# Kernel tuning notes

Measured on AMD Instinct MI355X. Metric: run time of the kernel, lower is better.

The kernel has to match this reference:

```python
import jax, jax.numpy as jnp
import numpy as np

B, N, C = 8, 4096, 768
H, M = 12, 64          # num_heads, num_landmarks
D = C // H             # head_dim = 64


def setup_inputs() -> dict:
    key = jax.random.key(0)
    k1, k2, k3, k4 = jax.random.split(key, 4)
    s = 0.02
    return {
        "x": jax.random.normal(k1, (B, N, C), dtype=jnp.float32),
        "w_qkv": jax.random.normal(k2, (3 * C, C), dtype=jnp.float32) * s,
        "w_proj": jax.random.normal(k3, (C, C), dtype=jnp.float32) * s,
        "b_proj": jax.random.normal(k4, (C,), dtype=jnp.float32) * s,
    }


def iterative_inv(mat, n_iter=6):
    # mat: [B, H, M, M]; Newton-Schulz cubic iteration for pseudo-inverse
    I = jnp.eye(mat.shape[-1], dtype=mat.dtype)
    K = mat
    # init: K^T / max_j(sum_i K_ij)  per (B,H)
    scale = jnp.max(jnp.sum(K, axis=-2), axis=-1)[:, :, None, None]
    V = jnp.swapaxes(K, -1, -2) / scale
    for _ in range(n_iter):
        KV = K @ V
        V = 0.25 * V @ (13.0 * I - KV @ (15.0 * I - KV @ (7.0 * I - KV)))
    return V


def reference(x, w_qkv, w_proj, b_proj):
    b, n, c = x.shape
    qkv = (x @ w_qkv.T).reshape(b, n, 3, H, D).transpose(2, 0, 3, 1, 4)  # [3,B,H,N,D]
    Q, K, V = qkv[0], qkv[1], qkv[2]
    Q = Q / (D ** 0.5)
    # landmark pooling (N % M == 0 path): segment means of length N//M
    Kl = K.reshape(b, H, M, n // M, D).mean(axis=-2)  # [B,H,M,D]
    Ql = Q.reshape(b, H, M, n // M, D).mean(axis=-2)  # [B,H,M,D]
    kernel1 = jax.nn.softmax(jnp.einsum('bhnd,bhmd->bhnm', Q, Kl), axis=-1)   # [B,H,N,M]
    kernel2 = jax.nn.softmax(jnp.einsum('bhmd,bhld->bhml', Ql, Kl), axis=-1)  # [B,H,M,M]
    kernel3 = jax.nn.softmax(jnp.einsum('bhmd,bhnd->bhmn', Ql, K), axis=-1)   # [B,H,M,N]
    SV = (kernel1 @ iterative_inv(kernel2)) @ (kernel3 @ V)  # [B,H,N,D]
    SV = SV.transpose(0, 2, 1, 3).reshape(b, n, c)
    out = SV @ w_proj.T + b_proj
    out = out + V.transpose(0, 2, 1, 3).reshape(b, n, c)
    return out
```

## Files before the change

### kernel.cpp

```cpp
#include <hip/hip_runtime.h>
#include <hip/hip_bf16.h>
#include <stdint.h>

typedef __bf16 bf16;
typedef __bf16 bf16x8 __attribute__((ext_vector_type(8)));
typedef __bf16 bf16x4 __attribute__((ext_vector_type(4)));
typedef float f32x4 __attribute__((ext_vector_type(4)));

#define B_ 8
#define N_ 4096
#define C_ 768
#define H_ 12
#define M_ 64
#define D_ 64
#define NT_ 32768
#define C3_ 2304

typedef __attribute__((address_space(3))) void lds_void_t;
typedef const __attribute__((address_space(1))) void gvoid_t;

__device__ __forceinline__ void gl_lds16(const void* gsrc, void* ldst) {
  __builtin_amdgcn_global_load_lds((gvoid_t*)(uintptr_t)gsrc,
                                   (lds_void_t*)(uintptr_t)ldst, 16, 0, 0);
}

__device__ __forceinline__ f32x4 mfma16(bf16x8 a, bf16x8 b, f32x4 c) {
  return __builtin_amdgcn_mfma_f32_16x16x32_bf16(a, b, c, 0, 0, 0);
}

#define VMW8 asm volatile("s_waitcnt vmcnt(8)" ::: "memory")
#define VMW4 asm volatile("s_waitcnt vmcnt(4)" ::: "memory")
#define VMW0 asm volatile("s_waitcnt vmcnt(0)" ::: "memory")
#define RAWBAR() { __builtin_amdgcn_sched_barrier(0); __builtin_amdgcn_s_barrier(); __builtin_amdgcn_sched_barrier(0); }

__global__ void k_cvt(const float* __restrict__ in, bf16* __restrict__ out, int n4) {
  const int stride = gridDim.x * blockDim.x;
  for (int i = blockIdx.x * blockDim.x + threadIdx.x; i < n4; i += stride) {
    f32x4 v = *(const f32x4*)(in + (size_t)i * 4);
    bf16x4 o;
    o[0] = (bf16)v[0]; o[1] = (bf16)v[1]; o[2] = (bf16)v[2]; o[3] = (bf16)v[3];
    *(bf16x4*)(out + (size_t)i * 4) = o;
  }
}

__global__ __launch_bounds__(512, 2) void k_qkv(
    const bf16* __restrict__ xbf, const bf16* __restrict__ wbf,
    bf16* __restrict__ Qb, bf16* __restrict__ Kb, bf16* __restrict__ Vb,
    float* __restrict__ Qlf, float* __restrict__ Klf)
{
  __shared__ bf16 As[4][8192];
  __shared__ bf16 Bs[4][8192];
  const int t = threadIdx.x;
  const int wave = t >> 6, lane = t & 63;
  const int l15 = lane & 15, l16 = lane >> 4;

  const int bid = blockIdx.x;
  const int swz = (bid & 7) * 144 + (bid >> 3);
  const int bt = swz / 9, ct = swz % 9;
  const int row0 = bt * 256, ct0 = ct * 256;
  const int wr = wave >> 2, wc = wave & 3;

  const int srow = t >> 2;
  const int scol = (((t & 3) ^ ((t >> 3) & 3)) << 3);
  const bf16* gaBase = xbf + (size_t)(row0 + srow) * C_ + scol;
  const bf16* gbBase = wbf + (size_t)(ct0 + srow) * C_ + scol;

  const int aoff = (wr * 128 + l15) * 32 + ((l16 ^ ((l15 >> 1) & 3)) << 3);
  const int boff = (wc * 64 + l15) * 32 + ((l16 ^ ((l15 >> 1) & 3)) << 3);

  f32x4 acc[8][4] = {};
  bf16x8 afr0[4], afr1[4], bfr[2][4];

#define QSTAGE(kt3) {                                                            \
    const int sb_ = (kt3) & 3;                                                   \
    gl_lds16(gaBase + (kt3) * 32, &As[sb_][t * 8]);                              \
    gl_lds16(gbBase + (kt3) * 32, &Bs[sb_][t * 8]);                              \
    gl_lds16(gaBase + (size_t)128 * C_ + (kt3) * 32, &As[sb_][(t + 512) * 8]);   \
    gl_lds16(gbBase + (size_t)128 * C_ + (kt3) * 32, &Bs[sb_][(t + 512) * 8]); }

#define QKSTEP(kt, DO_STAGE, DO_NXT, VMW_, DO_BAR) {                             \
    if (DO_STAGE) QSTAGE((kt) + 3);                                             \
    { const bf16* asC = As[(kt) & 3];                                            \
      _Pragma("unroll")                                                          \
      for (int i = 0; i < 4; ++i)                                                \
        afr1[i] = *(const bf16x8*)&asC[aoff + (4 + i) * 512]; }                  \
    __builtin_amdgcn_s_setprio(1);                                               \
    _Pragma("unroll")                                                            \
    for (int i = 0; i < 4; ++i)                                                  \
      _Pragma("unroll")                                                          \
      for (int j = 0; j < 4; ++j)                                                \
        acc[i][j] = mfma16(afr0[i], bfr[(kt) & 1][j], acc[i][j]);                \
    __builtin_amdgcn_s_setprio(0);                                               \
    if (DO_NXT) {                                                                \
      const bf16* asN = As[((kt) + 1) & 3];                                      \
      const bf16* bsN = Bs[((kt) + 1) & 3];                                      \
      _Pragma("unroll")                                                          \
      for (int i = 0; i < 4; ++i)                                                \
        afr0[i] = *(const bf16x8*)&asN[aoff + i * 512];                          \
      _Pragma("unroll")                                                          \
      for (int j = 0; j < 4; ++j)                                                \
        bfr[((kt) + 1) & 1][j] = *(const bf16x8*)&bsN[boff + j * 512]; }         \
    __builtin_amdgcn_s_setprio(1);                                               \
    _Pragma("unroll")                                                            \
    for (int i = 0; i < 4; ++i)                                                  \
      _Pragma("unroll")                                                          \
      for (int j = 0; j < 4; ++j)                                                \
        acc[4 + i][j] = mfma16(afr1[i], bfr[(kt) & 1][j], acc[4 + i][j]);        \
    __builtin_amdgcn_s_setprio(0);                                               \
    VMW_;                                                                        \
    if (DO_BAR) RAWBAR(); }

  QSTAGE(0); QSTAGE(1); QSTAGE(2);
  VMW4;
  RAWBAR();
#pragma unroll
  for (int i = 0; i < 4; ++i) afr0[i] = *(const bf16x8*)&As[0][aoff + i * 512];
#pragma unroll
  for (int j = 0; j < 4; ++j) bfr[0][j] = *(const bf16x8*)&Bs[0][boff + j * 512];

  QKSTEP(0, 1, 1, VMW4, 1)  QKSTEP(1, 1, 1, VMW4, 1)  QKSTEP(2, 1, 1, VMW4, 1)
  QKSTEP(3, 1, 1, VMW4, 1)  QKSTEP(4, 1, 1, VMW4, 1)  QKSTEP(5, 1, 1, VMW4, 1)
  QKSTEP(6, 1, 1, VMW4, 1)  QKSTEP(7, 1, 1, VMW4, 1)  QKSTEP(8, 1, 1, VMW4, 1)
  QKSTEP(9, 1, 1, VMW4, 1)  QKSTEP(10, 1, 1, VMW4, 1) QKSTEP(11, 1, 1, VMW4, 1)
  QKSTEP(12, 1, 1, VMW4, 1) QKSTEP(13, 1, 1, VMW4, 1) QKSTEP(14, 1, 1, VMW4, 1)
  QKSTEP(15, 1, 1, VMW4, 1) QKSTEP(16, 1, 1, VMW4, 1) QKSTEP(17, 1, 1, VMW4, 1)
  QKSTEP(18, 1, 1, VMW4, 1) QKSTEP(19, 1, 1, VMW4, 1) QKSTEP(20, 1, 1, VMW4, 1)
  QKSTEP(21, 0, 1, VMW0, 1)
  QKSTEP(22, 0, 1, (void)0, 1)
  QKSTEP(23, 0, 0, (void)0, 0)

#undef QKSTEP
#undef QSTAGE

  const int colblock = ct0 + wc * 64;
  const int which = colblock / C_;
  const int h = (colblock % C_) / D_;
  const int b = row0 >> 12;
  const int n_base = (row0 & (N_ - 1)) + wr * 128;
  bf16* dst = (which == 0) ? Qb : (which == 1) ? Kb : Vb;
  const float scale = (which == 0) ? 0.125f : 1.0f;
  const size_t base = ((size_t)(b * H_ + h) * N_ + n_base) * D_;
#pragma unroll
  for (int i = 0; i < 8; ++i)
#pragma unroll
    for (int q = 0; q < 4; ++q) {
      const int rloc = i * 16 + l16 * 4 + q;
#pragma unroll
      for (int j = 0; j < 4; ++j) {
        const int d = j * 16 + l15;
        dst[base + (size_t)rloc * D_ + d] = (bf16)(acc[i][j][q] * scale);
      }
    }
  if (which < 2) {
    float* lmout = (which == 0) ? Qlf : Klf;
#pragma unroll
    for (int g = 0; g < 2; ++g) {
      const int m = (n_base >> 6) + g;
#pragma unroll
      for (int j = 0; j < 4; ++j) {
        float s = 0.f;
#pragma unroll
        for (int i = 4 * g; i < 4 * g + 4; ++i)
#pragma unroll
          for (int q = 0; q < 4; ++q) s += acc[i][j][q];
        s *= scale;
        s += __shfl_xor(s, 16);
        s += __shfl_xor(s, 32);
        if (l16 == 0)
          lmout[((size_t)(b * H_ + h) * M_ + m) * D_ + j * 16 + lane] = s * (1.0f / 64.0f);
      }
    }
  }
}

__global__ __launch_bounds__(512, 1) void k_inv(
    const float* __restrict__ Qlf, const float* __restrict__ Klf,
    float* __restrict__ pinv, bf16* __restrict__ Qlb, bf16* __restrict__ Klb)
{
  __shared__ float K2[4096];
  __shared__ float Vm[4096];
  __shared__ float KV[4096];
  __shared__ float T1[4096];
  __shared__ float U1[4096];
  __shared__ float tmp64[64];
  __shared__ float sscale;
  const int t = threadIdx.x;
  const int bh = blockIdx.x;
  const size_t off = (size_t)bh * 4096;
  for (int idx = t; idx < 4096; idx += 512) {
    const float q = Qlf[off + idx];
    T1[idx] = q;
    Qlb[off + idx] = (bf16)q;
  }
  for (int idx = t; idx < 4096; idx += 512) {
    const int r = idx >> 6, c = idx & 63;
    const float k = Klf[off + idx];
    U1[c * 64 + r] = k;
    Klb[off + idx] = (bf16)k;
  }
  __syncthreads();
  const int j0 = (t & 15) * 4;
  const int i0 = (t >> 4) * 2;

  auto MMstep = [&](const float* A, const float* Bm, float* O, float dg, float sg, float al) {
    float r2[2][4] = {};
    for (int k = 0; k < 64; ++k) {
      f32x4 bv = *(const f32x4*)&Bm[k * 64 + j0];
      const float a0 = A[(i0 + 0) * 64 + k];
      const float a1 = A[(i0 + 1) * 64 + k];
#pragma unroll
      for (int jj = 0; jj < 4; ++jj) { r2[0][jj] += a0 * bv[jj]; r2[1][jj] += a1 * bv[jj]; }
    }
#pragma unroll
    for (int ii = 0; ii < 2; ++ii)
#pragma unroll
      for (int jj = 0; jj < 4; ++jj)
        O[(i0 + ii) * 64 + j0 + jj] = al * (dg * A[(i0 + ii) * 64 + (j0 + jj)] + sg * r2[ii][jj]);
    __syncthreads();
  };

  {
    float r2[2][4] = {};
    for (int k = 0; k < 64; ++k) {
      f32x4 bv = *(const f32x4*)&U1[k * 64 + j0];
      const float a0 = T1[(i0 + 0) * 64 + k];
      const float a1 = T1[(i0 + 1) * 64 + k];
#pragma unroll
      for (int jj = 0; jj < 4; ++jj) { r2[0][jj] += a0 * bv[jj]; r2[1][jj] += a1 * bv[jj]; }
    }
#pragma unroll
    for (int ii = 0; ii < 2; ++ii)
#pragma unroll
      for (int jj = 0; jj < 4; ++jj)
        K2[(i0 + ii) * 64 + j0 + jj] = __expf(r2[ii][jj]);
  }
  __syncthreads();
  if (t < 64) {
    float s = 0.f;
    for (int k = 0; k < 64; ++k) s += K2[t * 64 + k];
    tmp64[t] = 1.0f / s;
  }
  __syncthreads();
  for (int idx = t; idx < 4096; idx += 512) K2[idx] *= tmp64[idx >> 6];
  __syncthreads();
  if (t < 64) {
    float s = 0.f;
    for (int i = 0; i < 64; ++i) s += K2[i * 64 + t];
    tmp64[t] = s;
  }
  __syncthreads();
  if (t == 0) {
    float mx = tmp64[0];
    for (int j2 = 1; j2 < 64; ++j2) mx = fmaxf(mx, tmp64[j2]);
    sscale = 1.0f / mx;
  }
  __syncthreads();
  for (int idx = t; idx < 4096; idx += 512) {
    const int r = idx >> 6, c = idx & 63;
    Vm[idx] = K2[c * 64 + r] * sscale;
  }
  __syncthreads();

  float* pV = Vm;
  float* pT = T1;
  for (int it = 0; it < 6; ++it) {
    MMstep(K2, pV, KV, 0.f, 1.f, 1.f);
    MMstep(KV, KV, pT, 7.f, -1.f, 1.f);
    MMstep(KV, pT, U1, 15.f, -1.f, 1.f);
    MMstep(pV, U1, pT, 13.f, -1.f, 0.25f);
    float* sw = pV; pV = pT; pT = sw;
  }
  for (int idx = t; idx < 4096; idx += 512) pinv[off + idx] = pV[idx];
}

__global__ __launch_bounds__(256, 2) void k_k3v(
    const bf16* __restrict__ Qlb, const bf16* __restrict__ Kb, const bf16* __restrict__ Vb,
    float* __restrict__ Zacc, float* __restrict__ rowsum_g)
{
  __shared__ bf16 Qls[64 * 64];
  __shared__ bf16 Ks[128 * 64];
  __shared__ bf16 Vs[128 * 64];
  __shared__ bf16 Ps[64 * 128];
  __shared__ float rs[64];
  const int t = threadIdx.x, wave = t >> 6, lane = t & 63;
  const int bh = blockIdx.x >> 3;
  const int chunk = blockIdx.x & 7;
  const size_t kvbase = (size_t)bh * N_ * D_ + (size_t)chunk * 512 * D_;
  {
    const bf16* g = Qlb + (size_t)bh * 4096;
    gl_lds16(g + t * 8, &Qls[t * 8]);
    gl_lds16(g + (t + 256) * 8, &Qls[(t + 256) * 8]);
  }
  if (t < 64) rs[t] = 0.f;
  f32x4 z[4] = {};
  for (int st = 0; st < 4; ++st) {
    const bf16* gk = Kb + kvbase + (size_t)st * 128 * D_;
    const bf16* gv = Vb + kvbase + (size_t)st * 128 * D_;
#pragma unroll
    for (int c = 0; c < 4; ++c) {
      gl_lds16(gk + (t + c * 256) * 8, &Ks[(t + c * 256) * 8]);
      gl_lds16(gv + (t + c * 256) * 8, &Vs[(t + c * 256) * 8]);
    }
    __syncthreads();
    f32x4 sacc[4][2] = {};
#pragma unroll
    for (int kk = 0; kk < 2; ++kk) {
      bf16x8 af[4], bk[2];
#pragma unroll
      for (int i = 0; i < 4; ++i)
        af[i] = *(const bf16x8*)&Qls[(i * 16 + (lane & 15)) * 64 + kk * 32 + 8 * (lane >> 4)];
#pragma unroll
      for (int j2 = 0; j2 < 2; ++j2)
        bk[j2] = *(const bf16x8*)&Ks[(wave * 32 + j2 * 16 + (lane & 15)) * 64 + kk * 32 + 8 * (lane >> 4)];
#pragma unroll
      for (int i = 0; i < 4; ++i)
#pragma unroll
        for (int j2 = 0; j2 < 2; ++j2)
          sacc[i][j2] = mfma16(af[i], bk[j2], sacc[i][j2]);
    }
#pragma unroll
    for (int i = 0; i < 4; ++i)
#pragma unroll
      for (int q = 0; q < 4; ++q) {
        const float e0 = __expf(sacc[i][0][q]);
        const float e1 = __expf(sacc[i][1][q]);
        const int m = i * 16 + (lane >> 4) * 4 + q;
        Ps[m * 128 + wave * 32 + (lane & 15)] = (bf16)e0;
        Ps[m * 128 + wave * 32 + 16 + (lane & 15)] = (bf16)e1;
        float p = e0 + e1;
        p += __shfl_xor(p, 1); p += __shfl_xor(p, 2);
        p += __shfl_xor(p, 4); p += __shfl_xor(p, 8);
        if ((lane & 15) == 0) atomicAdd(&rs[m], p);
      }
    __syncthreads();
#pragma unroll
    for (int kk = 0; kk < 4; ++kk) {
      const int kbase = kk * 32 + 8 * (lane >> 4);
      const int d = wave * 16 + (lane & 15);
      bf16x8 bv;
#pragma unroll
      for (int e = 0; e < 8; ++e) bv[e] = Vs[(kbase + e) * 64 + d];
#pragma unroll
      for (int i = 0; i < 4; ++i) {
        bf16x8 ap = *(const bf16x8*)&Ps[(i * 16 + (lane & 15)) * 128 + kbase];
        z[i] = mfma16(ap, bv, z[i]);
      }
    }
    __syncthreads();
  }
  const size_t zbase = (size_t)bh * 4096;
#pragma unroll
  for (int i = 0; i < 4; ++i)
#pragma unroll
    for (int q = 0; q < 4; ++q) {
      const int m = i * 16 + (lane >> 4) * 4 + q;
      const int d = wave * 16 + (lane & 15);
      atomicAdd(&Zacc[zbase + m * 64 + d], z[i][q]);
    }
  if (t < 64) atomicAdd(&rowsum_g[bh * 64 + t], rs[t]);
}

__global__ __launch_bounds__(256, 1) void k_comb(
    const float* __restrict__ pinv, const float* __restrict__ Zacc,
    const float* __restrict__ rowsum_g, bf16* __restrict__ Wtb)
{
  __shared__ float Pv[4096];
  __shared__ float Zn[4096];
  const int t = threadIdx.x, bh = blockIdx.x;
  const size_t off = (size_t)bh * 4096;
  for (int idx = t; idx < 4096; idx += 256) Pv[idx] = pinv[off + idx];
  for (int idx = t; idx < 4096; idx += 256)
    Zn[idx] = Zacc[off + idx] / rowsum_g[bh * 64 + (idx >> 6)];
  __syncthreads();
  const int j0 = (t & 15) * 4, i0 = (t >> 4) * 4;
  float r[4][4] = {{0.f}};
  for (int k = 0; k < 64; ++k) {
    f32x4 bv = *(const f32x4*)&Zn[k * 64 + j0];
    float a[4];
#pragma unroll
    for (int ii = 0; ii < 4; ++ii) a[ii] = Pv[(i0 + ii) * 64 + k];
#pragma unroll
    for (int ii = 0; ii < 4; ++ii)
#pragma unroll
      for (int jj = 0; jj < 4; ++jj) r[ii][jj] += a[ii] * bv[jj];
  }
#pragma unroll
  for (int ii = 0; ii < 4; ++ii)
#pragma unroll
    for (int jj = 0; jj < 4; ++jj)
      Wtb[off + (size_t)(j0 + jj) * 64 + (i0 + ii)] = (bf16)r[ii][jj];
}

__global__ __launch_bounds__(256, 2) void k_sv(
    const bf16* __restrict__ Qb, const bf16* __restrict__ Klb,
    const bf16* __restrict__ Wtb, bf16* __restrict__ SVb)
{
  __shared__ bf16 Qs[128 * 64];
  __shared__ bf16 Kls[64 * 64];
  __shared__ bf16 Wts[64 * 64];
  __shared__ bf16 Ps[128 * 64];
  const int t = threadIdx.x, wave = t >> 6, lane = t & 63;
  const int bh = blockIdx.x >> 5;
  const int nt = blockIdx.x & 31;
  const int b = bh / H_, h = bh % H_;
  {
    const bf16* gq = Qb + (size_t)bh * N_ * D_ + (size_t)nt * 128 * D_;
#pragma unroll
    for (int c = 0; c < 4; ++c) gl_lds16(gq + (t + c * 256) * 8, &Qs[(t + c * 256) * 8]);
    const bf16* gkl = Klb + (size_t)bh * 4096;
    gl_lds16(gkl + t * 8, &Kls[t * 8]);
    gl_lds16(gkl + (t + 256) * 8, &Kls[(t + 256) * 8]);
    const bf16* gw = Wtb + (size_t)bh * 4096;
    gl_lds16(gw + t * 8, &Wts[t * 8]);
    gl_lds16(gw + (t + 256) * 8, &Wts[(t + 256) * 8]);
  }
  __syncthreads();
  f32x4 sacc[2][4] = {};
#pragma unroll
  for (int kk = 0; kk < 2; ++kk) {
    bf16x8 af[2], bl[4];
#pragma unroll
    for (int r = 0; r < 2; ++r)
      af[r] = *(const bf16x8*)&Qs[(wave * 32 + r * 16 + (lane & 15)) * 64 + kk * 32 + 8 * (lane >> 4)];
#pragma unroll
    for (int j = 0; j < 4; ++j)
      bl[j] = *(const bf16x8*)&Kls[(j * 16 + (lane & 15)) * 64 + kk * 32 + 8 * (lane >> 4)];
#pragma unroll
    for (int r = 0; r < 2; ++r)
#pragma unroll
      for (int j = 0; j < 4; ++j)
        sacc[r][j] = mfma16(af[r], bl[j], sacc[r][j]);
  }
#pragma unroll
  for (int r = 0; r < 2; ++r)
#pragma unroll
    for (int q = 0; q < 4; ++q) {
      float e[4]; float s = 0.f;
#pragma unroll
      for (int j = 0; j < 4; ++j) { e[j] = __expf(sacc[r][j][q]); s += e[j]; }
      s += __shfl_xor(s, 1); s += __shfl_xor(s, 2);
      s += __shfl_xor(s, 4); s += __shfl_xor(s, 8);
      const float is = 1.0f / s;
      const int row = wave * 32 + r * 16 + (lane >> 4) * 4 + q;
#pragma unroll
      for (int j = 0; j < 4; ++j)
        Ps[row * 64 + j * 16 + (lane & 15)] = (bf16)(e[j] * is);
    }
  __syncthreads();
  f32x4 oacc[2][4] = {};
#pragma unroll
  for (int kk = 0; kk < 2; ++kk) {
    bf16x8 af[2], bw[4];
#pragma unroll
    for (int r = 0; r < 2; ++r)
      af[r] = *(const bf16x8*)&Ps[(wave * 32 + r * 16 + (lane & 15)) * 64 + kk * 32 + 8 * (lane >> 4)];
#pragma unroll
    for (int j = 0; j < 4; ++j)
      bw[j] = *(const bf16x8*)&Wts[(j * 16 + (lane & 15)) * 64 + kk * 32 + 8 * (lane >> 4)];
#pragma unroll
    for (int r = 0; r < 2; ++r)
#pragma unroll
      for (int j = 0; j < 4; ++j)
        oacc[r][j] = mfma16(af[r], bw[j], oacc[r][j]);
  }
  const size_t outbase = ((size_t)b * N_ + (size_t)nt * 128) * C_ + h * 64;
#pragma unroll
  for (int r = 0; r < 2; ++r)
#pragma unroll
    for (int q = 0; q < 4; ++q) {
      const int row = wave * 32 + r * 16 + (lane >> 4) * 4 + q;
#pragma unroll
      for (int j = 0; j < 4; ++j)
        SVb[outbase + (size_t)row * C_ + j * 16 + (lane & 15)] = (bf16)(oacc[r][j][q]);
    }
}

__global__ __launch_bounds__(256, 2) void k_proj(
    const bf16* __restrict__ SVb, const bf16* __restrict__ wpb,
    const float* __restrict__ bproj, const bf16* __restrict__ Vb,
    float* __restrict__ outp)
{
  __shared__ bf16 As[4][4096];
  __shared__ bf16 Bs[4][4096];
  const int t = threadIdx.x;
  const int wave = t >> 6, lane = t & 63;
  const int l15 = lane & 15, l16 = lane >> 4;
  const int bid = blockIdx.x;
  const int swz = (bid & 7) * 192 + (bid >> 3);
  const int bt = swz / 6, ct = swz % 6;
  const int row0 = bt * 128, col0 = ct * 128;
  const int wr = wave >> 1, wc = wave & 1;

  const int srow = t >> 2;
  const int scol = (((t & 3) ^ ((t >> 3) & 3)) << 3);
  const bf16* ga = SVb + (size_t)(row0 + srow) * C_ + scol;
  const bf16* gb = wpb + (size_t)(col0 + srow) * C_ + scol;

  const int aoff = (wr * 64 + l15) * 32 + ((l16 ^ ((l15 >> 1) & 3)) << 3);
  const int boff = (wc * 64 + l15) * 32 + ((l16 ^ ((l15 >> 1) & 3)) << 3);

  f32x4 acc[4][4] = {};
  bf16x8 afr[2][4], bfr[2][4];

#define PSTAGE(kt3) {                                                          \
    const int sb_ = (kt3) & 3;                                                 \
    gl_lds16(ga + (kt3) * 32, &As[sb_][t * 8]);                                \
    gl_lds16(gb + (kt3) * 32, &Bs[sb_][t * 8]);                                \
    gl_lds16(ga + (size_t)64 * C_ + (kt3) * 32, &As[sb_][(t + 256) * 8]);      \
    gl_lds16(gb + (size_t)64 * C_ + (kt3) * 32, &Bs[sb_][(t + 256) * 8]); }

#define PKSTEP(kt, DO_STAGE, DO_NXT, VMW_, DO_BAR) {                           \
    if (DO_STAGE) PSTAGE((kt) + 3);                                            \
    if (DO_NXT) {                                                              \
      const bf16* asN = As[((kt) + 1) & 3];                                    \
      const bf16* bsN = Bs[((kt) + 1) & 3];                                    \
      _Pragma("unroll")                                                        \
      for (int i = 0; i < 4; ++i)                                              \
        afr[((kt) + 1) & 1][i] = *(const bf16x8*)&asN[aoff + i * 512];         \
      _Pragma("unroll")                                                        \
      for (int j = 0; j < 4; ++j)                                              \
        bfr[((kt) + 1) & 1][j] = *(const bf16x8*)&bsN[boff + j * 512]; }       \
    __builtin_amdgcn_s_setprio(1);                                             \
    _Pragma("unroll")                                                          \
    for (int i = 0; i < 4; ++i)                                                \
      _Pragma("unroll")                                                        \
      for (int j = 0; j < 4; ++j)                                              \
        acc[i][j] = mfma16(afr[(kt) & 1][i], bfr[(kt) & 1][j], acc[i][j]);     \
    __builtin_amdgcn_s_setprio(0);                                             \
    VMW_;                                                                      \
    if (DO_BAR) RAWBAR(); }

  PSTAGE(0); PSTAGE(1); PSTAGE(2);
  VMW4;
  RAWBAR();
#pragma unroll
  for (int i = 0; i < 4; ++i) afr[0][i] = *(const bf16x8*)&As[0][aoff + i * 512];
#pragma unroll
  for (int j = 0; j < 4; ++j) bfr[0][j] = *(const bf16x8*)&Bs[0][boff + j * 512];

  PKSTEP(0, 1, 1, VMW4, 1)  PKSTEP(1, 1, 1, VMW4, 1)  PKSTEP(2, 1, 1, VMW4, 1)
  PKSTEP(3, 1, 1, VMW4, 1)  PKSTEP(4, 1, 1, VMW4, 1)  PKSTEP(5, 1, 1, VMW4, 1)
  PKSTEP(6, 1, 1, VMW4, 1)  PKSTEP(7, 1, 1, VMW4, 1)  PKSTEP(8, 1, 1, VMW4, 1)
  PKSTEP(9, 1, 1, VMW4, 1)  PKSTEP(10, 1, 1, VMW4, 1) PKSTEP(11, 1, 1, VMW4, 1)
  PKSTEP(12, 1, 1, VMW4, 1) PKSTEP(13, 1, 1, VMW4, 1) PKSTEP(14, 1, 1, VMW4, 1)
  PKSTEP(15, 1, 1, VMW4, 1) PKSTEP(16, 1, 1, VMW4, 1) PKSTEP(17, 1, 1, VMW4, 1)
  PKSTEP(18, 1, 1, VMW4, 1) PKSTEP(19, 1, 1, VMW4, 1) PKSTEP(20, 1, 1, VMW4, 1)
  PKSTEP(21, 0, 1, VMW0, 1)
  PKSTEP(22, 0, 1, (void)0, 1)
  PKSTEP(23, 0, 0, (void)0, 0)

#undef PKSTEP
#undef PSTAGE

#pragma unroll
  for (int i = 0; i < 4; ++i)
#pragma unroll
    for (int q = 0; q < 4; ++q) {
      const int row = row0 + wr * 64 + i * 16 + l16 * 4 + q;
      const int b = row >> 12, n = row & (N_ - 1);
#pragma unroll
      for (int j = 0; j < 4; ++j) {
        const int col = col0 + wc * 64 + j * 16 + l15;
        const int h = col >> 6, d = col & 63;
        const float v = acc[i][j][q] + bproj[col] +
                        (float)Vb[((size_t)(b * H_ + h) * N_ + n) * D_ + d];
        outp[(size_t)row * C_ + col] = v;
      }
    }
}

extern "C" void kernel_launch(void* const* d_in, const int* in_sizes, int n_in,
                              void* d_out, int out_size, void* d_ws, size_t ws_size,
                              hipStream_t stream) {
  const float* x = (const float*)d_in[0];
  const float* wqkv = (const float*)d_in[1];
  const float* wproj = (const float*)d_in[2];
  const float* bproj = (const float*)d_in[3];
  float* outp = (float*)d_out;
  char* ws = (char*)d_ws;

  size_t off = 0;
  auto take = [&](size_t bytes) { char* p = ws + off; off += bytes; return p; };
  bf16* xbf     = (bf16*)take(50331648);
  bf16* wqkvbf  = (bf16*)take(3538944);
  bf16* wprojbf = (bf16*)take(1179648);
  bf16* Qb      = (bf16*)take(50331648);
  bf16* Kb      = (bf16*)take(50331648);
  bf16* Vb      = (bf16*)take(50331648);
  float* Qlf    = (float*)take(1572864);
  float* Klf    = (float*)take(1572864);
  bf16* Qlb     = (bf16*)take(786432);
  bf16* Klb     = (bf16*)take(786432);
  float* pinvp  = (float*)take(1572864);
  float* Zacc   = (float*)take(1572864);
  float* rowsum = (float*)take(24576);
  bf16* Wtb     = (bf16*)take(786432);
  bf16* SVb     = xbf;

  hipMemsetAsync(Zacc, 0, 1572864 + 24576, stream);

  k_cvt<<<2048, 256, 0, stream>>>(x, xbf, 25165824 / 4);
  k_cvt<<<432, 256, 0, stream>>>(wqkv, wqkvbf, 1769472 / 4);
  k_cvt<<<144, 256, 0, stream>>>(wproj, wprojbf, 589824 / 4);
  k_qkv<<<1152, 512, 0, stream>>>(xbf, wqkvbf, Qb, Kb, Vb, Qlf, Klf);
  k_inv<<<96, 512, 0, stream>>>(Qlf, Klf, pinvp, Qlb, Klb);
  k_k3v<<<768, 256, 0, stream>>>(Qlb, Kb, Vb, Zacc, rowsum);
  k_comb<<<96, 256, 0, stream>>>(pinvp, Zacc, rowsum, Wtb);
  k_sv<<<96 * 32, 256, 0, stream>>>(Qb, Klb, Wtb, SVb);
  k_proj<<<1536, 256, 0, stream>>>(SVb, wprojbf, bproj, Vb, outp);
}
```

Before: 388.6 us.

## Restructure QKV GEMM main loop to BK=64 double-buffered quadrant schedule

Result: no change. 392.0 us (+0.9%).

```diff
diff --git a/kernel.cpp b/kernel.cpp
--- a/kernel.cpp
+++ b/kernel.cpp
@@ -31,6 +31,7 @@
 #define VMW8 asm volatile("s_waitcnt vmcnt(8)" ::: "memory")
 #define VMW4 asm volatile("s_waitcnt vmcnt(4)" ::: "memory")
 #define VMW0 asm volatile("s_waitcnt vmcnt(0)" ::: "memory")
+#define LGKM0 asm volatile("s_waitcnt lgkmcnt(0)" ::: "memory")
 #define RAWBAR() { __builtin_amdgcn_sched_barrier(0); __builtin_amdgcn_s_barrier(); __builtin_amdgcn_sched_barrier(0); }
 
 __global__ void k_cvt(const float* __restrict__ in, bf16* __restrict__ out, int n4) {
@@ -48,8 +49,8 @@
     bf16* __restrict__ Qb, bf16* __restrict__ Kb, bf16* __restrict__ Vb,
     float* __restrict__ Qlf, float* __restrict__ Klf)
 {
-  __shared__ bf16 As[4][8192];
-  __shared__ bf16 Bs[4][8192];
+  __shared__ bf16 As[2][16384];
+  __shared__ bf16 Bs[2][16384];
   const int t = threadIdx.x;
   const int wave = t >> 6, lane = t & 63;
   const int l15 = lane & 15, l16 = lane >> 4;
@@ -60,77 +61,89 @@
   const int row0 = bt * 256, ct0 = ct * 256;
   const int wr = wave >> 2, wc = wave & 3;
 
-  const int srow = t >> 2;
-  const int scol = (((t & 3) ^ ((t >> 3) & 3)) << 3);
+  const int srow = t >> 3;
+  const int scol = (((t >> 2) & 1) << 5) | (((t & 3) ^ ((t >> 4) & 3)) << 3);
   const bf16* gaBase = xbf + (size_t)(row0 + srow) * C_ + scol;
   const bf16* gbBase = wbf + (size_t)(ct0 + srow) * C_ + scol;
 
-  const int aoff = (wr * 128 + l15) * 32 + ((l16 ^ ((l15 >> 1) & 3)) << 3);
-  const int boff = (wc * 64 + l15) * 32 + ((l16 ^ ((l15 >> 1) & 3)) << 3);
+  const int xorv = (l15 >> 1) & 3;
+  const int aoff = (wr * 128 + l15) * 64 + ((l16 ^ xorv) << 3);
+  const int boff = (wc * 64 + l15) * 64 + ((l16 ^ xorv) << 3);
 
   f32x4 acc[8][4] = {};
-  bf16x8 afr0[4], afr1[4], bfr[2][4];
-
-#define QSTAGE(kt3) {                                                            \
-    const int sb_ = (kt3) & 3;                                                   \
-    gl_lds16(gaBase + (kt3) * 32, &As[sb_][t * 8]);                              \
-    gl_lds16(gbBase + (kt3) * 32, &Bs[sb_][t * 8]);                              \
-    gl_lds16(gaBase + (size_t)128 * C_ + (kt3) * 32, &As[sb_][(t + 512) * 8]);   \
-    gl_lds16(gbBase + (size_t)128 * C_ + (kt3) * 32, &Bs[sb_][(t + 512) * 8]); }
-
-#define QKSTEP(kt, DO_STAGE, DO_NXT, VMW_, DO_BAR) {                             \
-    if (DO_STAGE) QSTAGE((kt) + 3);                                             \
-    { const bf16* asC = As[(kt) & 3];                                            \
-      _Pragma("unroll")                                                          \
-      for (int i = 0; i < 4; ++i)                                                \
-        afr1[i] = *(const bf16x8*)&asC[aoff + (4 + i) * 512]; }                  \
-    __builtin_amdgcn_s_setprio(1);                                               \
-    _Pragma("unroll")                                                            \
-    for (int i = 0; i < 4; ++i)                                                  \
-      _Pragma("unroll")                                                          \
-      for (int j = 0; j < 4; ++j)                                                \
-        acc[i][j] = mfma16(afr0[i], bfr[(kt) & 1][j], acc[i][j]);                \
-    __builtin_amdgcn_s_setprio(0);                                               \
-    if (DO_NXT) {                                                                \
-      const bf16* asN = As[((kt) + 1) & 3];                                      \
-      const bf16* bsN = Bs[((kt) + 1) & 3];                                      \
-      _Pragma("unroll")                                                          \
-      for (int i = 0; i < 4; ++i)                                                \
-        afr0[i] = *(const bf16x8*)&asN[aoff + i * 512];                          \
-      _Pragma("unroll")                                                          \
-      for (int j = 0; j < 4; ++j)                                                \
-        bfr[((kt) + 1) & 1][j] = *(const bf16x8*)&bsN[boff + j * 512]; }         \
-    __builtin_amdgcn_s_setprio(1);                                               \
-    _Pragma("unroll")                                                            \
-    for (int i = 0; i < 4; ++i)                                                  \
-      _Pragma("unroll")                                                          \
-      for (int j = 0; j < 4; ++j)                                                \
-        acc[4 + i][j] = mfma16(afr1[i], bfr[(kt) & 1][j], acc[4 + i][j]);        \
-    __builtin_amdgcn_s_setprio(0);                                               \
-    VMW_;                                                                        \
-    if (DO_BAR) RAWBAR(); }
-
-  QSTAGE(0); QSTAGE(1); QSTAGE(2);
-  VMW4;
+  bf16x8 afr[4][2], bc0[2][2], bc1[2][2];
+
+#define STG_A(tt, c) gl_lds16(gaBase + (size_t)((c) * 64) * C_ + (tt) * 64, &As[(tt) & 1][(c) * 4096 + t * 8])
+#define STG_B(tt, c) gl_lds16(gbBase + (size_t)((c) * 64) * C_ + (tt) * 64, &Bs[(tt) & 1][(c) * 4096 + t * 8])
+
+#define MFMAQ(RH, CH, BREG) {                                                          \
+    __builtin_amdgcn_s_setprio(1);                                                    \
+    _Pragma("unroll")                                                                  \
+    for (int f = 0; f < 4; ++f) {                                                      \
+      acc[(RH)*4+f][(CH)*2+0] = mfma16(afr[f][0], BREG[0][0], acc[(RH)*4+f][(CH)*2+0]);\
+      acc[(RH)*4+f][(CH)*2+0] = mfma16(afr[f][1], BREG[0][1], acc[(RH)*4+f][(CH)*2+0]);\
+      acc[(RH)*4+f][(CH)*2+1] = mfma16(afr[f][0], BREG[1][0], acc[(RH)*4+f][(CH)*2+1]);\
+      acc[(RH)*4+f][(CH)*2+1] = mfma16(afr[f][1], BREG[1][1], acc[(RH)*4+f][(CH)*2+1]);\
+    }                                                                                  \
+    __builtin_amdgcn_s_setprio(0); }
+
+#define QTILE(T, DOSTG, VMQ) {                                                         \
+    const bf16* as_ = As[(T) & 1];                                                     \
+    const bf16* bs_ = Bs[(T) & 1];                                                     \
+                                                       \
+    _Pragma("unroll")                                                                  \
+    for (int f = 0; f < 4; ++f) {                                                      \
+      afr[f][0] = *(const bf16x8*)&as_[aoff + (f * 16) * 64];                          \
+      afr[f][1] = *(const bf16x8*)&as_[aoff + (f * 16) * 64 + 32]; }                   \
+    _Pragma("unroll")                                                                  \
+    for (int cf = 0; cf < 2; ++cf) {                                                   \
+      bc0[cf][0] = *(const bf16x8*)&bs_[boff + (cf * 16) * 64];                        \
+      bc0[cf][1] = *(const bf16x8*)&bs_[boff + (cf * 16) * 64 + 32]; }                 \
+    RAWBAR(); LGKM0;                                                                   \
+    MFMAQ(0, 0, bc0)                                                                   \
+    RAWBAR();                                                                          \
+                                        \
+    _Pragma("unroll")                                                                  \
+    for (int cf = 0; cf < 2; ++cf) {                                                   \
+      bc1[cf][0] = *(const bf16x8*)&bs_[boff + (32 + cf * 16) * 64];                   \
+      bc1[cf][1] = *(const bf16x8*)&bs_[boff + (32 + cf * 16) * 64 + 32]; }            \
+    if (DOSTG) { STG_A((T) + 2, 0); STG_A((T) + 2, 2); }                               \
+    RAWBAR(); LGKM0;                                                                   \
+    MFMAQ(0, 1, bc1)                                                                   \
+    RAWBAR();                                                                          \
+                                                    \
+    _Pragma("unroll")                                                                  \
+    for (int f = 0; f < 4; ++f) {                                                      \
+      afr[f][0] = *(const bf16x8*)&as_[aoff + (64 + f * 16) * 64];                     \
+      afr[f][1] = *(const bf16x8*)&as_[aoff + (64 + f * 16) * 64 + 32]; }              \
+    if (DOSTG) { STG_B((T) + 2, 0); STG_B((T) + 2, 1); }                               \
+    RAWBAR(); LGKM0;                                                                   \
+    MFMAQ(1, 1, bc1)                                                                   \
+    RAWBAR();                                                                          \
+                          \
+    if (DOSTG) { STG_A((T) + 2, 1); STG_A((T) + 2, 3); STG_B((T) + 2, 2); STG_B((T) + 2, 3); } \
+    RAWBAR();                                                                          \
+    MFMAQ(1, 0, bc0)                                                                   \
+    VMQ;                                                                               \
+    RAWBAR(); }
+
+  STG_A(0, 0); STG_A(0, 1); STG_A(0, 2); STG_A(0, 3);
+  STG_B(0, 0); STG_B(0, 1); STG_B(0, 2); STG_B(0, 3);
+  STG_A(1, 0); STG_A(1, 1); STG_A(1, 2); STG_A(1, 3);
+  STG_B(1, 0); STG_B(1, 1); STG_B(1, 2); STG_B(1, 3);
+  VMW8;
   RAWBAR();
-#pragma unroll
-  for (int i = 0; i < 4; ++i) afr0[i] = *(const bf16x8*)&As[0][aoff + i * 512];
-#pragma unroll
-  for (int j = 0; j < 4; ++j) bfr[0][j] = *(const bf16x8*)&Bs[0][boff + j * 512];
-
-  QKSTEP(0, 1, 1, VMW4, 1)  QKSTEP(1, 1, 1, VMW4, 1)  QKSTEP(2, 1, 1, VMW4, 1)
-  QKSTEP(3, 1, 1, VMW4, 1)  QKSTEP(4, 1, 1, VMW4, 1)  QKSTEP(5, 1, 1, VMW4, 1)
-  QKSTEP(6, 1, 1, VMW4, 1)  QKSTEP(7, 1, 1, VMW4, 1)  QKSTEP(8, 1, 1, VMW4, 1)
-  QKSTEP(9, 1, 1, VMW4, 1)  QKSTEP(10, 1, 1, VMW4, 1) QKSTEP(11, 1, 1, VMW4, 1)
-  QKSTEP(12, 1, 1, VMW4, 1) QKSTEP(13, 1, 1, VMW4, 1) QKSTEP(14, 1, 1, VMW4, 1)
-  QKSTEP(15, 1, 1, VMW4, 1) QKSTEP(16, 1, 1, VMW4, 1) QKSTEP(17, 1, 1, VMW4, 1)
-  QKSTEP(18, 1, 1, VMW4, 1) QKSTEP(19, 1, 1, VMW4, 1) QKSTEP(20, 1, 1, VMW4, 1)
-  QKSTEP(21, 0, 1, VMW0, 1)
-  QKSTEP(22, 0, 1, (void)0, 1)
-  QKSTEP(23, 0, 0, (void)0, 0)
-
-#undef QKSTEP
-#undef QSTAGE
+
+  QTILE(0, 1, VMW8)  QTILE(1, 1, VMW8)  QTILE(2, 1, VMW8)  QTILE(3, 1, VMW8)
+  QTILE(4, 1, VMW8)  QTILE(5, 1, VMW8)  QTILE(6, 1, VMW8)  QTILE(7, 1, VMW8)
+  QTILE(8, 1, VMW8)  QTILE(9, 1, VMW8)
+  QTILE(10, 0, VMW0)
+  QTILE(11, 0, (void)0)
+
+#undef QTILE
+#undef MFMAQ
+#undef STG_A
+#undef STG_B
 
   const int colblock = ct0 + wc * 64;
   const int which = colblock / C_;
```

## Fold landmark weights into per-batch projection matrix and fuse softmax with projection

Applied to the files above, without the earlier changes.

Result: slower. 434.5 us (+11.8%).

```diff
diff --git a/kernel.cpp b/kernel.cpp
--- a/kernel.cpp
+++ b/kernel.cpp
@@ -360,211 +360,173 @@
   if (t < 64) atomicAdd(&rowsum_g[bh * 64 + t], rs[t]);
 }
 
-__global__ __launch_bounds__(256, 1) void k_comb(
+__global__ __launch_bounds__(256, 2) void k_comb2(
     const float* __restrict__ pinv, const float* __restrict__ Zacc,
-    const float* __restrict__ rowsum_g, bf16* __restrict__ Wtb)
+    const float* __restrict__ rowsum_g, const bf16* __restrict__ wpb,
+    bf16* __restrict__ WcombT)
 {
   __shared__ float Pv[4096];
   __shared__ float Zn[4096];
+  __shared__ bf16 Wl[4096];
   const int t = threadIdx.x, bh = blockIdx.x;
+  const int b = bh / H_, h = bh % H_;
   const size_t off = (size_t)bh * 4096;
   for (int idx = t; idx < 4096; idx += 256) Pv[idx] = pinv[off + idx];
   for (int idx = t; idx < 4096; idx += 256)
     Zn[idx] = Zacc[off + idx] / rowsum_g[bh * 64 + (idx >> 6)];
   __syncthreads();
-  const int j0 = (t & 15) * 4, i0 = (t >> 4) * 4;
-  float r[4][4] = {{0.f}};
-  for (int k = 0; k < 64; ++k) {
-    f32x4 bv = *(const f32x4*)&Zn[k * 64 + j0];
-    float a[4];
-#pragma unroll
-    for (int ii = 0; ii < 4; ++ii) a[ii] = Pv[(i0 + ii) * 64 + k];
+  {
+    const int j0 = (t & 15) * 4, i0 = (t >> 4) * 4;
+    float r[4][4] = {{0.f}};
+    for (int k = 0; k < 64; ++k) {
+      f32x4 bv = *(const f32x4*)&Zn[k * 64 + j0];
+      float a[4];
+#pragma unroll
+      for (int ii = 0; ii < 4; ++ii) a[ii] = Pv[(i0 + ii) * 64 + k];
+#pragma unroll
+      for (int ii = 0; ii < 4; ++ii)
+#pragma unroll
+        for (int jj = 0; jj < 4; ++jj) r[ii][jj] += a[ii] * bv[jj];
+    }
 #pragma unroll
     for (int ii = 0; ii < 4; ++ii)
 #pragma unroll
-      for (int jj = 0; jj < 4; ++jj) r[ii][jj] += a[ii] * bv[jj];
-  }
-#pragma unroll
-  for (int ii = 0; ii < 4; ++ii)
-#pragma unroll
-    for (int jj = 0; jj < 4; ++jj)
-      Wtb[off + (size_t)(j0 + jj) * 64 + (i0 + ii)] = (bf16)r[ii][jj];
-}
-
-__global__ __launch_bounds__(256, 2) void k_sv(
-    const bf16* __restrict__ Qb, const bf16* __restrict__ Klb,
-    const bf16* __restrict__ Wtb, bf16* __restrict__ SVb)
-{
-  __shared__ bf16 Qs[128 * 64];
-  __shared__ bf16 Kls[64 * 64];
-  __shared__ bf16 Wts[64 * 64];
-  __shared__ bf16 Ps[128 * 64];
-  const int t = threadIdx.x, wave = t >> 6, lane = t & 63;
-  const int bh = blockIdx.x >> 5;
-  const int nt = blockIdx.x & 31;
-  const int b = bh / H_, h = bh % H_;
-  {
-    const bf16* gq = Qb + (size_t)bh * N_ * D_ + (size_t)nt * 128 * D_;
-#pragma unroll
-    for (int c = 0; c < 4; ++c) gl_lds16(gq + (t + c * 256) * 8, &Qs[(t + c * 256) * 8]);
-    const bf16* gkl = Klb + (size_t)bh * 4096;
-    gl_lds16(gkl + t * 8, &Kls[t * 8]);
-    gl_lds16(gkl + (t + 256) * 8, &Kls[(t + 256) * 8]);
-    const bf16* gw = Wtb + (size_t)bh * 4096;
-    gl_lds16(gw + t * 8, &Wts[t * 8]);
-    gl_lds16(gw + (t + 256) * 8, &Wts[(t + 256) * 8]);
-  }
-  __syncthreads();
-  f32x4 sacc[2][4] = {};
-#pragma unroll
-  for (int kk = 0; kk < 2; ++kk) {
-    bf16x8 af[2], bl[4];
-#pragma unroll
-    for (int r = 0; r < 2; ++r)
-      af[r] = *(const bf16x8*)&Qs[(wave * 32 + r * 16 + (lane & 15)) * 64 + kk * 32 + 8 * (lane >> 4)];
-#pragma unroll
-    for (int j = 0; j < 4; ++j)
-      bl[j] = *(const bf16x8*)&Kls[(j * 16 + (lane & 15)) * 64 + kk * 32 + 8 * (lane >> 4)];
-#pragma unroll
-    for (int r = 0; r < 2; ++r)
-#pragma unroll
-      for (int j = 0; j < 4; ++j)
-        sacc[r][j] = mfma16(af[r], bl[j], sacc[r][j]);
-  }
-#pragma unroll
-  for (int r = 0; r < 2; ++r)
-#pragma unroll
-    for (int q = 0; q < 4; ++q) {
-      float e[4]; float s = 0.f;
-#pragma unroll
-      for (int j = 0; j < 4; ++j) { e[j] = __expf(sacc[r][j][q]); s += e[j]; }
-      s += __shfl_xor(s, 1); s += __shfl_xor(s, 2);
-      s += __shfl_xor(s, 4); s += __shfl_xor(s, 8);
-      const float is = 1.0f / s;
-      const int row = wave * 32 + r * 16 + (lane >> 4) * 4 + q;
-#pragma unroll
-      for (int j = 0; j < 4; ++j)
-        Ps[row * 64 + j * 16 + (lane & 15)] = (bf16)(e[j] * is);
-    }
-  __syncthreads();
-  f32x4 oacc[2][4] = {};
-#pragma unroll
-  for (int kk = 0; kk < 2; ++kk) {
-    bf16x8 af[2], bw[4];
-#pragma unroll
-    for (int r = 0; r < 2; ++r)
-      af[r] = *(const bf16x8*)&Ps[(wave * 32 + r * 16 + (lane & 15)) * 64 + kk * 32 + 8 * (lane >> 4)];
-#pragma unroll
-    for (int j = 0; j < 4; ++j)
-      bw[j] = *(const bf16x8*)&Wts[(j * 16 + (lane & 15)) * 64 + kk * 32 + 8 * (lane >> 4)];
-#pragma unroll
-    for (int r = 0; r < 2; ++r)
-#pragma unroll
-      for (int j = 0; j < 4; ++j)
-        oacc[r][j] = mfma16(af[r], bw[j], oacc[r][j]);
-  }
-  const size_t outbase = ((size_t)b * N_ + (size_t)nt * 128) * C_ + h * 64;
-#pragma unroll
-  for (int r = 0; r < 2; ++r)
-#pragma unroll
-    for (int q = 0; q < 4; ++q) {
-      const int row = wave * 32 + r * 16 + (lane >> 4) * 4 + q;
-#pragma unroll
-      for (int j = 0; j < 4; ++j)
-        SVb[outbase + (size_t)row * C_ + j * 16 + (lane & 15)] = (bf16)(oacc[r][j][q]);
-    }
-}
-
-__global__ __launch_bounds__(256, 2) void k_proj(
-    const bf16* __restrict__ SVb, const bf16* __restrict__ wpb,
-    const float* __restrict__ bproj, const bf16* __restrict__ Vb,
-    float* __restrict__ outp)
-{
-  __shared__ bf16 As[4][4096];
-  __shared__ bf16 Bs[4][4096];
-  const int t = threadIdx.x;
+      for (int jj = 0; jj < 4; ++jj) {
+        const int m = i0 + ii, d = j0 + jj;
+        Wl[m * 64 + ((((d >> 3) ^ (m & 7)) << 3) | (d & 7))] = (bf16)r[ii][jj];
+      }
+  }
+  __syncthreads();
   const int wave = t >> 6, lane = t & 63;
   const int l15 = lane & 15, l16 = lane >> 4;
-  const int bid = blockIdx.x;
-  const int swz = (bid & 7) * 192 + (bid >> 3);
-  const int bt = swz / 6, ct = swz % 6;
-  const int row0 = bt * 128, col0 = ct * 128;
-  const int wr = wave >> 1, wc = wave & 1;
-
-  const int srow = t >> 2;
-  const int scol = (((t & 3) ^ ((t >> 3) & 3)) << 3);
-  const bf16* ga = SVb + (size_t)(row0 + srow) * C_ + scol;
-  const bf16* gb = wpb + (size_t)(col0 + srow) * C_ + scol;
-
-  const int aoff = (wr * 64 + l15) * 32 + ((l16 ^ ((l15 >> 1) & 3)) << 3);
-  const int boff = (wc * 64 + l15) * 32 + ((l16 ^ ((l15 >> 1) & 3)) << 3);
-
-  f32x4 acc[4][4] = {};
-  bf16x8 afr[2][4], bfr[2][4];
-
-#define PSTAGE(kt3) {                                                          \
-    const int sb_ = (kt3) & 3;                                                 \
-    gl_lds16(ga + (kt3) * 32, &As[sb_][t * 8]);                                \
-    gl_lds16(gb + (kt3) * 32, &Bs[sb_][t * 8]);                                \
-    gl_lds16(ga + (size_t)64 * C_ + (kt3) * 32, &As[sb_][(t + 256) * 8]);      \
-    gl_lds16(gb + (size_t)64 * C_ + (kt3) * 32, &Bs[sb_][(t + 256) * 8]); }
-
-#define PKSTEP(kt, DO_STAGE, DO_NXT, VMW_, DO_BAR) {                           \
-    if (DO_STAGE) PSTAGE((kt) + 3);                                            \
-    if (DO_NXT) {                                                              \
-      const bf16* asN = As[((kt) + 1) & 3];                                    \
-      const bf16* bsN = Bs[((kt) + 1) & 3];                                    \
-      _Pragma("unroll")                                                        \
-      for (int i = 0; i < 4; ++i)                                              \
-        afr[((kt) + 1) & 1][i] = *(const bf16x8*)&asN[aoff + i * 512];         \
-      _Pragma("unroll")                                                        \
-      for (int j = 0; j < 4; ++j)                                              \
-        bfr[((kt) + 1) & 1][j] = *(const bf16x8*)&bsN[boff + j * 512]; }       \
-    __builtin_amdgcn_s_setprio(1);                                             \
-    _Pragma("unroll")                                                          \
-    for (int i = 0; i < 4; ++i)                                                \
-      _Pragma("unroll")                                                        \
-      for (int j = 0; j < 4; ++j)                                              \
-        acc[i][j] = mfma16(afr[(kt) & 1][i], bfr[(kt) & 1][j], acc[i][j]);     \
-    __builtin_amdgcn_s_setprio(0);                                             \
-    VMW_;                                                                      \
-    if (DO_BAR) RAWBAR(); }
-
-  PSTAGE(0); PSTAGE(1); PSTAGE(2);
-  VMW4;
-  RAWBAR();
-#pragma unroll
-  for (int i = 0; i < 4; ++i) afr[0][i] = *(const bf16x8*)&As[0][aoff + i * 512];
-#pragma unroll
-  for (int j = 0; j < 4; ++j) bfr[0][j] = *(const bf16x8*)&Bs[0][boff + j * 512];
-
-  PKSTEP(0, 1, 1, VMW4, 1)  PKSTEP(1, 1, 1, VMW4, 1)  PKSTEP(2, 1, 1, VMW4, 1)
-  PKSTEP(3, 1, 1, VMW4, 1)  PKSTEP(4, 1, 1, VMW4, 1)  PKSTEP(5, 1, 1, VMW4, 1)
-  PKSTEP(6, 1, 1, VMW4, 1)  PKSTEP(7, 1, 1, VMW4, 1)  PKSTEP(8, 1, 1, VMW4, 1)
-  PKSTEP(9, 1, 1, VMW4, 1)  PKSTEP(10, 1, 1, VMW4, 1) PKSTEP(11, 1, 1, VMW4, 1)
-  PKSTEP(12, 1, 1, VMW4, 1) PKSTEP(13, 1, 1, VMW4, 1) PKSTEP(14, 1, 1, VMW4, 1)
-  PKSTEP(15, 1, 1, VMW4, 1) PKSTEP(16, 1, 1, VMW4, 1) PKSTEP(17, 1, 1, VMW4, 1)
-  PKSTEP(18, 1, 1, VMW4, 1) PKSTEP(19, 1, 1, VMW4, 1) PKSTEP(20, 1, 1, VMW4, 1)
-  PKSTEP(21, 0, 1, VMW0, 1)
-  PKSTEP(22, 0, 1, (void)0, 1)
-  PKSTEP(23, 0, 0, (void)0, 0)
-
-#undef PKSTEP
-#undef PSTAGE
-
+  const bf16* wpr = wpb + h * 64;
+  bf16* outb = WcombT + (size_t)b * C_ * C_ + h * 64;
+#pragma unroll
+  for (int g = 0; g < 3; ++g) {
+    f32x4 a2[4][4] = {};
+#pragma unroll
+    for (int kk = 0; kk < 2; ++kk) {
+      bf16x8 afw[4], bfw[4];
+#pragma unroll
+      for (int tt = 0; tt < 4; ++tt) {
+        const int c2 = wave * 192 + (g * 4 + tt) * 16 + l15;
+        afw[tt] = *(const bf16x8*)(wpr + (size_t)c2 * C_ + kk * 32 + 8 * l16);
+      }
+#pragma unroll
+      for (int mt = 0; mt < 4; ++mt) {
+        const int m = mt * 16 + l15;
+        bfw[mt] = *(const bf16x8*)&Wl[m * 64 + (((kk * 4 + l16) ^ (m & 7)) << 3)];
+      }
+#pragma unroll
+      for (int tt = 0; tt < 4; ++tt)
+#pragma unroll
+        for (int mt = 0; mt < 4; ++mt)
+          a2[tt][mt] = mfma16(afw[tt], bfw[mt], a2[tt][mt]);
+    }
+#pragma unroll
+    for (int tt = 0; tt < 4; ++tt)
+#pragma unroll
+      for (int q = 0; q < 4; ++q) {
+        const int c2 = wave * 192 + (g * 4 + tt) * 16 + l16 * 4 + q;
+#pragma unroll
+        for (int mt = 0; mt < 4; ++mt)
+          outb[(size_t)c2 * C_ + mt * 16 + l15] = (bf16)a2[tt][mt][q];
+      }
+  }
+}
+
+__global__ __launch_bounds__(512, 1) void k_svp(
+    const bf16* __restrict__ Qb, const bf16* __restrict__ Klb,
+    const bf16* __restrict__ WcombT, const float* __restrict__ bproj,
+    const bf16* __restrict__ Vb, float* __restrict__ outp)
+{
+  __shared__ bf16 P[64 * 768];
+  const int t = threadIdx.x, wave = t >> 6, lane = t & 63;
+  const int l15 = lane & 15, l16 = lane >> 4;
+  const int b = blockIdx.x & 7;
+  const int rt = blockIdx.x >> 3;
+  const int n0 = rt * 64;
+
+#pragma unroll
+  for (int hh = 0; hh < 2; ++hh) {
+    const int h = wave + hh * 8;
+    if (hh == 0 || wave < 4) {
+      const int bh = b * H_ + h;
+      const bf16* q = Qb + ((size_t)bh * N_ + n0) * D_;
+      const bf16* kl = Klb + (size_t)bh * 4096;
+      f32x4 s4[4][4] = {};
+#pragma unroll
+      for (int kk = 0; kk < 2; ++kk) {
+        bf16x8 af[4], bf_[4];
+#pragma unroll
+        for (int i = 0; i < 4; ++i)
+          af[i] = *(const bf16x8*)(q + (size_t)(i * 16 + l15) * D_ + kk * 32 + 8 * l16);
+#pragma unroll
+        for (int j = 0; j < 4; ++j)
+          bf_[j] = *(const bf16x8*)(kl + (size_t)(j * 16 + l15) * D_ + kk * 32 + 8 * l16);
+#pragma unroll
+        for (int i = 0; i < 4; ++i)
+#pragma unroll
+          for (int j = 0; j < 4; ++j)
+            s4[i][j] = mfma16(af[i], bf_[j], s4[i][j]);
+      }
+#pragma unroll
+      for (int i = 0; i < 4; ++i)
+#pragma unroll
+        for (int q2 = 0; q2 < 4; ++q2) {
+          float e[4]; float s = 0.f;
+#pragma unroll
+          for (int j = 0; j < 4; ++j) { e[j] = __expf(s4[i][j][q2]); s += e[j]; }
+          s += __shfl_xor(s, 1); s += __shfl_xor(s, 2);
+          s += __shfl_xor(s, 4); s += __shfl_xor(s, 8);
+          const float is = 1.0f / s;
+          const int row = i * 16 + l16 * 4 + q2;
+#pragma unroll
+          for (int j = 0; j < 4; ++j) {
+            const int col = j * 16 + l15;
+            P[row * 768 + h * 64 + ((((col >> 3) ^ (row & 7)) << 3) | (col & 7))] =
+                (bf16)(e[j] * is);
+          }
+        }
+    }
+  }
+  __syncthreads();
+
+  const bf16* wct = WcombT + (size_t)b * C_ * C_;
+  f32x4 oa[4][6] = {};
+  for (int ch = 0; ch < 12; ++ch) {
+#pragma unroll
+    for (int kk = 0; kk < 2; ++kk) {
+      bf16x8 ap[4], bw[6];
+#pragma unroll
+      for (int i = 0; i < 4; ++i) {
+        const int row = i * 16 + l15;
+        ap[i] = *(const bf16x8*)&P[row * 768 + ch * 64 + (((kk * 4 + l16) ^ (row & 7)) << 3)];
+      }
+#pragma unroll
+      for (int j = 0; j < 6; ++j) {
+        const int c2 = wave * 96 + j * 16 + l15;
+        bw[j] = *(const bf16x8*)(wct + (size_t)c2 * C_ + ch * 64 + kk * 32 + 8 * l16);
+      }
+#pragma unroll
+      for (int i = 0; i < 4; ++i)
+#pragma unroll
+        for (int j = 0; j < 6; ++j)
+          oa[i][j] = mfma16(ap[i], bw[j], oa[i][j]);
+    }
+  }
 #pragma unroll
   for (int i = 0; i < 4; ++i)
 #pragma unroll
-    for (int q = 0; q < 4; ++q) {
-      const int row = row0 + wr * 64 + i * 16 + l16 * 4 + q;
-      const int b = row >> 12, n = row & (N_ - 1);
-#pragma unroll
-      for (int j = 0; j < 4; ++j) {
-        const int col = col0 + wc * 64 + j * 16 + l15;
-        const int h = col >> 6, d = col & 63;
-        const float v = acc[i][j][q] + bproj[col] +
-                        (float)Vb[((size_t)(b * H_ + h) * N_ + n) * D_ + d];
-        outp[(size_t)row * C_ + col] = v;
+    for (int q2 = 0; q2 < 4; ++q2) {
+      const int n = n0 + i * 16 + l16 * 4 + q2;
+#pragma unroll
+      for (int j = 0; j < 6; ++j) {
+        const int col = wave * 96 + j * 16 + l15;
+        const int h2 = col >> 6, d = col & 63;
+        const float v = oa[i][j][q2] + bproj[col] +
+                        (float)Vb[((size_t)(b * H_ + h2) * N_ + n) * D_ + d];
+        outp[((size_t)b * N_ + n) * C_ + col] = v;
       }
     }
 }
@@ -594,8 +556,7 @@
   float* pinvp  = (float*)take(1572864);
   float* Zacc   = (float*)take(1572864);
   float* rowsum = (float*)take(24576);
-  bf16* Wtb     = (bf16*)take(786432);
-  bf16* SVb     = xbf;
+  bf16* WcombT  = (bf16*)take(9437184);
 
   hipMemsetAsync(Zacc, 0, 1572864 + 24576, stream);
 
@@ -605,7 +566,6 @@
   k_qkv<<<1152, 512, 0, stream>>>(xbf, wqkvbf, Qb, Kb, Vb, Qlf, Klf);
   k_inv<<<96, 512, 0, stream>>>(Qlf, Klf, pinvp, Qlb, Klb);
   k_k3v<<<768, 256, 0, stream>>>(Qlb, Kb, Vb, Zacc, rowsum);
-  k_comb<<<96, 256, 0, stream>>>(pinvp, Zacc, rowsum, Wtb);
-  k_sv<<<96 * 32, 256, 0, stream>>>(Qb, Klb, Wtb, SVb);
-  k_proj<<<1536, 256, 0, stream>>>(SVb, wprojbf, bproj, Vb, outp);
-}
+  k_comb2<<<96, 256, 0, stream>>>(pinvp, Zacc, rowsum, wprojbf, WcombT);
+  k_svp<<<512, 512, 0, stream>>>(Qb, Klb, WcombT, bproj, Vb, outp);
+}
```
